# Performance work log

Measured on AMD Instinct MI355X. Metric: run time of the kernel, lower is better.

Reference implementation:

```python
import jax, jax.numpy as jnp
import numpy as np

NUM_TAGS = 256
BATCH = 64
SEQ = 512


def setup_inputs() -> dict:
    key = jax.random.key(0)
    k1, k2, k3 = jax.random.split(key, 3)
    logits = jax.random.normal(k1, (BATCH, SEQ, NUM_TAGS), dtype=jnp.float32)
    tags = jax.random.randint(k2, (BATCH, SEQ), 0, NUM_TAGS, dtype=jnp.int32)
    mask = jnp.ones((BATCH, SEQ), dtype=jnp.int32)
    # learned parameter: transitions [K, K] (xavier-normal-ish init)
    std = float(np.sqrt(2.0 / (NUM_TAGS + NUM_TAGS)))
    transitions = jax.random.normal(k3, (NUM_TAGS, NUM_TAGS), dtype=jnp.float32) * std
    return {"logits": logits, "tags": tags, "mask": mask, "transitions": transitions}


def _input_likelihood(logits, mask, transitions):
    # logits: [B, S, K], mask: [B, S] float
    logits_t = jnp.transpose(logits, (1, 0, 2))  # [S, B, K]
    mask_t = jnp.transpose(mask, (1, 0))         # [S, B]
    alpha0 = logits_t[0]                          # [B, K]

    def step(alpha, xs):
        logit_i, mask_i = xs                      # [B, K], [B]
        # inner: [B, K_prev, K_next]
        inner = alpha[:, :, None] + logit_i[:, None, :] + transitions[None, :, :]
        new_alpha = jax.nn.logsumexp(inner, axis=1)
        m = mask_i[:, None]
        alpha = new_alpha * m + alpha * (1.0 - m)
        return alpha, None

    alpha, _ = jax.lax.scan(step, alpha0, (logits_t[1:], mask_t[1:]))
    return jax.nn.logsumexp(alpha, axis=-1)      # [B]


def _joint_likelihood(logits, tags, mask, transitions):
    # logits: [B, S, K], tags: [B, S] int, mask: [B, S] float
    B, S, K = logits.shape
    # transition scores for steps 0..S-2 -> transitions[tags[i], tags[i+1]] * mask[i+1]
    trans = transitions[tags[:, :-1], tags[:, 1:]] * mask[:, 1:]      # [B, S-1]
    # emit scores for steps 0..S-2 -> logits[i, tags[i]] * mask[i]
    emit = jnp.take_along_axis(logits[:, :-1], tags[:, :-1, None], axis=-1)[..., 0] * mask[:, :-1]
    score = trans.sum(axis=1) + emit.sum(axis=1)                      # [B]
    # last valid tag per batch (mask is a contiguous prefix)
    last_idx = mask.sum(axis=1).astype(jnp.int32) - 1                 # [B]
    last_tags = jnp.take_along_axis(tags, last_idx[:, None], axis=1)[:, 0]
    last_input = logits[:, -1, :][jnp.arange(B), last_tags]           # [B]
    score = score + last_input * mask[:, -1]
    return score


def reference(logits, tags, mask, transitions):
    mask_f = mask.astype(logits.dtype)
    log_num = _joint_likelihood(logits, tags, mask_f, transitions)
    log_den = _input_likelihood(logits, mask_f, transitions)
    return jnp.sum(log_num - log_den)
```

## Files before the change

kernel.cpp:

```cpp
#include <hip/hip_runtime.h>
#include <stdint.h>

#define NTAGS 256
#define BATCH 64
#define SEQ   512
#define MB    16
#define NTHREADS 512

typedef __attribute__((ext_vector_type(8))) short short8;
typedef __attribute__((ext_vector_type(4))) float f32x4;

__device__ __forceinline__ unsigned int f32_to_bf16_bits(float f) {
  unsigned int u = __float_as_uint(f);
  return (u + 0x7FFFu + ((u >> 16) & 1u)) >> 16;
}
__device__ __forceinline__ float wave_sum(float v) {
#pragma unroll
  for (int o = 32; o; o >>= 1) v += __shfl_xor(v, o);
  return v;
}
__device__ __forceinline__ unsigned int pk_bf16(float lo, float hi) {
  unsigned int r;
  asm("v_cvt_pk_bf16_f32 %0, %1, %2" : "=v"(r) : "v"(lo), "v"(hi));
  return r;
}

#define LOG2E 1.4426950408889634f

#define BAR_LGKM() \
    asm volatile("s_waitcnt lgkmcnt(0)" ::: "memory"); \
    __builtin_amdgcn_s_barrier(); \
    asm volatile("" ::: "memory");

#define MFMA_ALL(RB) \
    f32x4 acc0 = {0.f,0.f,0.f,0.f}, acc1 = {0.f,0.f,0.f,0.f}; \
    _Pragma("unroll") \
    for (int c = 0; c < 8; ++c) { \
      const short8 bf = *(const short8*)&alds[RB][bidxs[c]]; \
      acc0 = __builtin_amdgcn_mfma_f32_16x16x32_bf16(aF[0][c], bf, acc0, 0, 0, 0); \
      acc1 = __builtin_amdgcn_mfma_f32_16x16x32_bf16(aF[1][c], bf, acc1, 0, 0, 0); \
    }

#define EPI_TILE_F(I, ACCI, PB, WB, ME) { \
      const uint2 pw = PB[I]; \
      const float p0_ = __uint_as_float(pw.x << 16); \
      const float p1_ = __uint_as_float(pw.x & 0xFFFF0000u); \
      const float p2_ = __uint_as_float(pw.y << 16); \
      const float p3_ = __uint_as_float(pw.y & 0xFFFF0000u); \
      const float n0 = (MM ? ACCI[0] * p0_ : sOld[I][0]) * sc; \
      const float n1 = (MM ? ACCI[1] * p1_ : sOld[I][1]) * sc; \
      const float n2 = (MM ? ACCI[2] * p2_ : sOld[I][2]) * sc; \
      const float n3 = (MM ? ACCI[3] * p3_ : sOld[I][3]) * sc; \
      sOld[I][0] = n0; sOld[I][1] = n1; sOld[I][2] = n2; sOld[I][3] = n3; \
      if (ME) mxl = fmaxf(mxl, fmaxf(fmaxf(n0, n1), fmaxf(n2, n3))); \
      uint2 wv; wv.x = pk_bf16(n0, n1); wv.y = pk_bf16(n2, n3); \
      *(uint2*)&alds[WB][widx[I]] = wv; }

#define EPI_TILE_B(I, ACCI, PB, WB, ME) { \
      const uint2 pw = PB[I]; \
      const float p0_ = __uint_as_float(pw.x << 16); \
      const float p1_ = __uint_as_float(pw.x & 0xFFFF0000u); \
      const float p2_ = __uint_as_float(pw.y << 16); \
      const float p3_ = __uint_as_float(pw.y & 0xFFFF0000u); \
      float n0, n1, n2, n3; \
      if (fastm) { \
        n0 = ACCI[0] * p0_ * sc; n1 = ACCI[1] * p1_ * sc; \
        n2 = ACCI[2] * p2_ * sc; n3 = ACCI[3] * p3_ * sc; \
      } else { \
        const float q0_ = __uint_as_float(gp[I].x << 16); \
        const float q1_ = __uint_as_float(gp[I].x & 0xFFFF0000u); \
        const float q2_ = __uint_as_float(gp[I].y << 16); \
        const float q3_ = __uint_as_float(gp[I].y & 0xFFFF0000u); \
        n0 = (MM ? ACCI[0] * p0_ : sOld[I][0] * (p0_ / q0_)) * sc; \
        n1 = (MM ? ACCI[1] * p1_ : sOld[I][1] * (p1_ / q1_)) * sc; \
        n2 = (MM ? ACCI[2] * p2_ : sOld[I][2] * (p2_ / q2_)) * sc; \
        n3 = (MM ? ACCI[3] * p3_ : sOld[I][3] * (p3_ / q3_)) * sc; \
      } \
      gp[I] = pw; \
      sOld[I][0] = n0; sOld[I][1] = n1; sOld[I][2] = n2; sOld[I][3] = n3; \
      if (ME) mxl = fmaxf(mxl, fmaxf(fmaxf(n0, n1), fmaxf(n2, n3))); \
      uint2 wv; wv.x = pk_bf16(n0, n1); wv.y = pk_bf16(n2, n3); \
      *(uint2*)&alds[WB][widx[I]] = wv; }

#define APPLY_BODY() { \
      const f32x4 mxa = *(const f32x4*)&maxw[p][0]; \
      const f32x4 mxb = *(const f32x4*)&maxw[p][4]; \
      const float mx = fmaxf(fmaxf(fmaxf(mxa[0], mxa[1]), fmaxf(mxa[2], mxa[3])), \
                             fmaxf(fmaxf(mxb[0], mxb[1]), fmaxf(mxb[2], mxb[3]))); \
      const int e = (int)((__float_as_uint(mx) >> 23) & 0xFF) - 127; \
      esum += e; \
      sc = __uint_as_float((unsigned int)(127 - e) << 23); }

#define STEPF(T, RB, WB, PC, PL, MC, ML, APPLY, MEAS) { \
    { const int tp_ = ((T) + 2 < SEQ) ? ((T) + 2) : (SEQ - 1); \
      _Pragma("unroll") \
      for (int i2 = 0; i2 < 2; ++i2) PL[i2] = *(const uint2*)(Pp + (size_t)tp_ * NTAGS + 16 * i2); \
      ML = mkp[tp_]; } \
    MFMA_ALL(RB) \
    float sc = 1.0f; \
    if (APPLY) APPLY_BODY() \
    const int MM = MC; \
    float mxl = -3.0e38f; \
    EPI_TILE_F(0, acc0, PC, WB, MEAS) EPI_TILE_F(1, acc1, PC, WB, MEAS) \
    if (MEAS) { \
      float v = mxl; v = fmaxf(v, __shfl_xor(v, 16)); v = fmaxf(v, __shfl_xor(v, 32)); \
      if (q == 0) maxw[p][wid] = v; \
    } \
    BAR_LGKM() }

#define STEPB(T, RB, WB, PC, PL, MC, ML, APPLY, MEAS) { \
    { const int tp_ = ((T) >= 2) ? ((T) - 2) : 0; \
      const int tm_ = ((T) >= 1) ? ((T) - 1) : 0; \
      _Pragma("unroll") \
      for (int i2 = 0; i2 < 2; ++i2) PL[i2] = *(const uint2*)(Pp + (size_t)tp_ * NTAGS + 16 * i2); \
      ML = mkp[tm_]; } \
    MFMA_ALL(RB) \
    float sc = 1.0f; \
    if (APPLY) APPLY_BODY() \
    const int MM = MC; \
    const bool fastm = (bool)__all(MM != 0); \
    float mxl = -3.0e38f; \
    EPI_TILE_B(0, acc0, PC, WB, MEAS) EPI_TILE_B(1, acc1, PC, WB, MEAS) \
    if (MEAS) { \
      float v = mxl; v = fmaxf(v, __shfl_xor(v, 16)); v = fmaxf(v, __shfl_xor(v, 32)); \
      if (q == 0) maxw[p][wid] = v; \
    } \
    BAR_LGKM() }

__global__ __launch_bounds__(256)
void crf_prep(const float* __restrict__ lg, unsigned int* __restrict__ P)
{
  const size_t g = (size_t)blockIdx.x * 256 + threadIdx.x;
  const float4 a = ((const float4*)lg)[2 * g];
  const float4 b = ((const float4*)lg)[2 * g + 1];
  uint4 o;
  o.x = pk_bf16(exp2f(a.x * LOG2E), exp2f(a.y * LOG2E));
  o.y = pk_bf16(exp2f(a.z * LOG2E), exp2f(a.w * LOG2E));
  o.z = pk_bf16(exp2f(b.x * LOG2E), exp2f(b.y * LOG2E));
  o.w = pk_bf16(exp2f(b.z * LOG2E), exp2f(b.w * LOG2E));
  ((uint4*)P)[g] = o;
}

__global__ __launch_bounds__(NTHREADS, 2)
void crf_halves(const unsigned short* __restrict__ P,
                const int*   __restrict__ mask,
                const float* __restrict__ trans,
                float* __restrict__ wsA, float* __restrict__ wsB,
                int* __restrict__ wseF, int* __restrict__ wseB)
{
  const int bid  = blockIdx.x;
  const int bwd  = bid >> 2;
  const int b0   = (bid & 3) * MB;
  const int tid  = threadIdx.x;
  const int wid  = tid >> 6;
  const int lane = tid & 63;
  const int p    = lane & 15;
  const int q    = lane >> 4;

  __shared__ __align__(16) short alds[2][NTAGS * MB];
  __shared__ __align__(32) float maxw[16][8];

  const unsigned short* Pp = P + (size_t)(b0 + p) * SEQ * NTAGS + 32 * wid + 4 * q;
  const int* mkp = mask + (b0 + p) * SEQ;

  int bidxs[8], widx[2];
#pragma unroll
  for (int c = 0; c < 8; ++c) bidxs[c] = (p * NTAGS + 32 * c + 8 * q) ^ ((p & 7) << 3);
#pragma unroll
  for (int i = 0; i < 2; ++i) widx[i] = (p * NTAGS + 32 * wid + 16 * i + 4 * q) ^ ((p & 7) << 3);

  short8 aF[2][8];
#pragma unroll
  for (int i = 0; i < 2; ++i) {
    const int m = 32 * wid + 16 * i + p;
#pragma unroll
    for (int c = 0; c < 8; ++c) {
      short8 w;
#pragma unroll
      for (int j = 0; j < 8; ++j) {
        const int tag = 32 * c + 8 * q + j;
        const float tv = bwd ? trans[m * NTAGS + tag] : trans[tag * NTAGS + m];
        w[j] = (short)f32_to_bf16_bits(exp2f(tv * LOG2E));
      }
      aF[i][c] = w;
    }
  }

  f32x4 sOld[2];
  uint2 p0[2], p1[2], p2[2], p3[2], gp[2];
  int m0 = 1, m1 = 1, m2 = 1, m3 = 1;
  int esum = 0;

  if (!bwd) {
#pragma unroll
    for (int i = 0; i < 2; ++i) {
      const uint2 pw = *(const uint2*)(Pp + 16 * i);
      f32x4 a;
      a[0] = __uint_as_float(pw.x << 16); a[1] = __uint_as_float(pw.x & 0xFFFF0000u);
      a[2] = __uint_as_float(pw.y << 16); a[3] = __uint_as_float(pw.y & 0xFFFF0000u);
      sOld[i] = a;
      *(uint2*)&alds[0][widx[i]] = pw;
    }
#pragma unroll
    for (int i = 0; i < 2; ++i) {
      p1[i] = *(const uint2*)(Pp + 1 * NTAGS + 16 * i);
      p2[i] = *(const uint2*)(Pp + 2 * NTAGS + 16 * i);
    }
    m1 = mkp[1]; m2 = mkp[2];
    __syncthreads();

    STEPF(1, 0, 1, p1, p3, m1, m3, 0, 0)
    STEPF(2, 1, 0, p2, p0, m2, m0, 0, 0)
    STEPF(3, 0, 1, p3, p1, m3, m1, 0, 1)
#pragma unroll 1
    for (int tb = 4; tb <= 248; tb += 4) {
      STEPF(tb + 0, 1, 0, p0, p2, m0, m2, 1, 0)
      STEPF(tb + 1, 0, 1, p1, p3, m1, m3, 0, 0)
      STEPF(tb + 2, 1, 0, p2, p0, m2, m0, 0, 0)
      STEPF(tb + 3, 0, 1, p3, p1, m3, m1, 0, 1)
    }
    STEPF(252, 1, 0, p0, p2, m0, m2, 1, 0)
    STEPF(253, 0, 1, p1, p3, m1, m3, 0, 0)
    STEPF(254, 1, 0, p2, p0, m2, m0, 0, 0)

    {
      MFMA_ALL(0)
      const int MM = m3;
      float* wp = wsA + (size_t)(b0 + p) * NTAGS + 32 * wid + 4 * q;
#pragma unroll
      for (int i = 0; i < 2; ++i) {
        const uint2 pw = p3[i];
        f32x4 pv;
        pv[0] = __uint_as_float(pw.x << 16); pv[1] = __uint_as_float(pw.x & 0xFFFF0000u);
        pv[2] = __uint_as_float(pw.y << 16); pv[3] = __uint_as_float(pw.y & 0xFFFF0000u);
        f32x4 o;
        const f32x4 ac = (i == 0) ? acc0 : acc1;
#pragma unroll
        for (int r = 0; r < 4; ++r)
          o[r] = MM ? ac[r] * pv[r] : sOld[i][r];
        *(f32x4*)(wp + 16 * i) = o;
      }
    }
    if (tid < 16) wseF[b0 + tid] = esum;
  } else {
#pragma unroll
    for (int i = 0; i < 2; ++i) {
      const uint2 pw = *(const uint2*)(Pp + (size_t)(SEQ - 1) * NTAGS + 16 * i);
      f32x4 a;
      a[0] = __uint_as_float(pw.x << 16); a[1] = __uint_as_float(pw.x & 0xFFFF0000u);
      a[2] = __uint_as_float(pw.y << 16); a[3] = __uint_as_float(pw.y & 0xFFFF0000u);
      sOld[i] = a; gp[i] = pw;
      *(uint2*)&alds[0][widx[i]] = pw;
    }
#pragma unroll
    for (int i = 0; i < 2; ++i) {
      p2[i] = *(const uint2*)(Pp + (size_t)510 * NTAGS + 16 * i);
      p1[i] = *(const uint2*)(Pp + (size_t)509 * NTAGS + 16 * i);
    }
    m2 = mkp[511];
    m1 = mkp[510];
    __syncthreads();

    STEPB(510, 0, 1, p2, p0, m2, m0, 0, 0)
    STEPB(509, 1, 0, p1, p3, m1, m3, 0, 0)
    STEPB(508, 0, 1, p0, p2, m0, m2, 0, 1)
#pragma unroll 1
    for (int tb = 507; tb >= 263; tb -= 4) {
      STEPB(tb - 0, 1, 0, p3, p1, m3, m1, 1, 0)
      STEPB(tb - 1, 0, 1, p2, p0, m2, m0, 0, 0)
      STEPB(tb - 2, 1, 0, p1, p3, m1, m3, 0, 0)
      STEPB(tb - 3, 0, 1, p0, p2, m0, m2, 0, 1)
    }
    STEPB(259, 1, 0, p3, p1, m3, m1, 1, 0)
    STEPB(258, 0, 1, p2, p0, m2, m0, 0, 0)
    STEPB(257, 1, 0, p1, p3, m1, m3, 0, 0)
    STEPB(256, 0, 1, p0, p2, m0, m2, 0, 0)

    {
      MFMA_ALL(1)
      float* wp = wsB + (size_t)(b0 + p) * NTAGS + 32 * wid + 4 * q;
      *(f32x4*)(wp + 0)  = acc0;
      *(f32x4*)(wp + 16) = acc1;
    }
    if (tid < 16) wseB[b0 + tid] = esum;
  }
}

__global__ __launch_bounds__(256)
void crf_combine(const float* __restrict__ logits,
                 const int*   __restrict__ tags,
                 const int*   __restrict__ mask,
                 const float* __restrict__ trans,
                 const float* __restrict__ wsA,
                 const float* __restrict__ wsB,
                 const int*   __restrict__ wseF,
                 const int*   __restrict__ wseB,
                 float* __restrict__ out)
{
  const int b    = blockIdx.x;
  const int tid  = threadIdx.x;
  const int lane = tid & 63;
  const int wid  = tid >> 6;

  __shared__ float rn[4], rm[4], rp[4];

  const float LN2 = 0.6931471805599453f;
  const float* lg = logits + (size_t)b * SEQ * NTAGS;
  const int*   tg = tags + b * SEQ;
  const int*   mk = mask + b * SEQ;

  float numer = 0.f, msum = 0.f;
  for (int t = tid; t < SEQ; t += 256) {
    int   tag_t = tg[t];
    float m_t   = (float)mk[t];
    msum += m_t;
    if (t < SEQ - 1) {
      numer += lg[t * NTAGS + tag_t] * m_t;
      numer += trans[tag_t * NTAGS + tg[t + 1]] * (float)mk[t + 1];
    }
  }
  numer = wave_sum(numer);
  msum  = wave_sum(msum);
  if (lane == 0) { rn[wid] = numer; rm[wid] = msum; }

  float pprod = wsA[b * NTAGS + tid] * wsB[b * NTAGS + tid];
  pprod = wave_sum(pprod);
  if (lane == 0) rp[wid] = pprod;
  __syncthreads();

  if (tid == 0) {
    const float numer_tot = (rn[0] + rn[1]) + (rn[2] + rn[3]);
    const float msum_tot  = (rm[0] + rm[1]) + (rm[2] + rm[3]);
    const float psum      = (rp[0] + rp[1]) + (rp[2] + rp[3]);
    const float log_den   = logf(psum) + (float)(wseF[b] + wseB[b]) * LN2;
    int last_idx = (int)msum_tot - 1;
    if (last_idx < 0) last_idx = 0;
    const int last_tag = tg[last_idx];
    const float score = numer_tot + lg[(SEQ - 1) * NTAGS + last_tag] * (float)mk[SEQ - 1];
    atomicAdd(out, score - log_den);
  }
}

extern "C" void kernel_launch(void* const* d_in, const int* in_sizes, int n_in,
                              void* d_out, int out_size, void* d_ws, size_t ws_size,
                              hipStream_t stream) {
  const float* logits = (const float*)d_in[0];
  const int*   tags   = (const int*)d_in[1];
  const int*   mask   = (const int*)d_in[2];
  const float* trans  = (const float*)d_in[3];
  float* out = (float*)d_out;

  unsigned short* P = (unsigned short*)d_ws;
  float* wsA  = (float*)((char*)d_ws + (size_t)BATCH * SEQ * NTAGS * 2);
  float* wsB  = wsA + BATCH * NTAGS;
  int*   wseF = (int*)(wsB + BATCH * NTAGS);
  int*   wseB = wseF + BATCH;

  hipMemsetAsync(out, 0, sizeof(float), stream);
  crf_prep<<<dim3(BATCH * SEQ * NTAGS / (256 * 8)), dim3(256), 0, stream>>>(logits, (unsigned int*)P);
  crf_halves<<<dim3(8), dim3(NTHREADS), 0, stream>>>(P, mask, trans, wsA, wsB, wseF, wseB);
  crf_combine<<<dim3(BATCH), dim3(256), 0, stream>>>(logits, tags, mask, trans, wsA, wsB, wseF, wseB, out);
}
```

Baseline: 280.1 us.

## Split recurrence across more blocks with four batch rows per block

Each crf_halves block now handles 4 batch rows instead of 16, so the launch grows from 8 to 32 blocks. Inside the 16-wide MFMA N dimension the rows are replicated, and only lanes with p<4 write LDS, the max buffer and outputs. The LDS swizzle is adapted to the smaller buffer. The aim is to shorten the latency-bound sequential chain per block by using more CUs, at the cost of redundant MFMA work and loading the transition matrix in more blocks.

```diff
diff --git a/kernel.cpp b/kernel.cpp
--- a/kernel.cpp
+++ b/kernel.cpp
@@ -4,7 +4,7 @@
 #define NTAGS 256
 #define BATCH 64
 #define SEQ   512
-#define MB    16
+#define BR    4
 #define NTHREADS 512
 
 typedef __attribute__((ext_vector_type(8))) short short8;
@@ -54,7 +54,7 @@
       sOld[I][0] = n0; sOld[I][1] = n1; sOld[I][2] = n2; sOld[I][3] = n3; \
       if (ME) mxl = fmaxf(mxl, fmaxf(fmaxf(n0, n1), fmaxf(n2, n3))); \
       uint2 wv; wv.x = pk_bf16(n0, n1); wv.y = pk_bf16(n2, n3); \
-      *(uint2*)&alds[WB][widx[I]] = wv; }
+      if (wrt) *(uint2*)&alds[WB][widx[I]] = wv; }
 
 #define EPI_TILE_B(I, ACCI, PB, WB, ME) { \
       const uint2 pw = PB[I]; \
@@ -80,11 +80,11 @@
       sOld[I][0] = n0; sOld[I][1] = n1; sOld[I][2] = n2; sOld[I][3] = n3; \
       if (ME) mxl = fmaxf(mxl, fmaxf(fmaxf(n0, n1), fmaxf(n2, n3))); \
       uint2 wv; wv.x = pk_bf16(n0, n1); wv.y = pk_bf16(n2, n3); \
-      *(uint2*)&alds[WB][widx[I]] = wv; }
+      if (wrt) *(uint2*)&alds[WB][widx[I]] = wv; }
 
 #define APPLY_BODY() { \
-      const f32x4 mxa = *(const f32x4*)&maxw[p][0]; \
-      const f32x4 mxb = *(const f32x4*)&maxw[p][4]; \
+      const f32x4 mxa = *(const f32x4*)&maxw[pc][0]; \
+      const f32x4 mxb = *(const f32x4*)&maxw[pc][4]; \
       const float mx = fmaxf(fmaxf(fmaxf(mxa[0], mxa[1]), fmaxf(mxa[2], mxa[3])), \
                              fmaxf(fmaxf(mxb[0], mxb[1]), fmaxf(mxb[2], mxb[3]))); \
       const int e = (int)((__float_as_uint(mx) >> 23) & 0xFF) - 127; \
@@ -104,7 +104,7 @@
     EPI_TILE_F(0, acc0, PC, WB, MEAS) EPI_TILE_F(1, acc1, PC, WB, MEAS) \
     if (MEAS) { \
       float v = mxl; v = fmaxf(v, __shfl_xor(v, 16)); v = fmaxf(v, __shfl_xor(v, 32)); \
-      if (q == 0) maxw[p][wid] = v; \
+      if (q == 0 && wrt) maxw[p][wid] = v; \
     } \
     BAR_LGKM() }
 
@@ -123,7 +123,7 @@
     EPI_TILE_B(0, acc0, PC, WB, MEAS) EPI_TILE_B(1, acc1, PC, WB, MEAS) \
     if (MEAS) { \
       float v = mxl; v = fmaxf(v, __shfl_xor(v, 16)); v = fmaxf(v, __shfl_xor(v, 32)); \
-      if (q == 0) maxw[p][wid] = v; \
+      if (q == 0 && wrt) maxw[p][wid] = v; \
     } \
     BAR_LGKM() }
 
@@ -149,25 +149,27 @@
                 int* __restrict__ wseF, int* __restrict__ wseB)
 {
   const int bid  = blockIdx.x;
-  const int bwd  = bid >> 2;
-  const int b0   = (bid & 3) * MB;
+  const int bwd  = bid >> 4;
+  const int b0   = (bid & 15) * BR;
   const int tid  = threadIdx.x;
   const int wid  = tid >> 6;
   const int lane = tid & 63;
   const int p    = lane & 15;
+  const int pc   = p & (BR - 1);
   const int q    = lane >> 4;
-
-  __shared__ __align__(16) short alds[2][NTAGS * MB];
-  __shared__ __align__(32) float maxw[16][8];
-
-  const unsigned short* Pp = P + (size_t)(b0 + p) * SEQ * NTAGS + 32 * wid + 4 * q;
-  const int* mkp = mask + (b0 + p) * SEQ;
+  const bool wrt = (p < BR);
+
+  __shared__ __align__(16) short alds[2][NTAGS * BR];
+  __shared__ __align__(32) float maxw[BR][8];
+
+  const unsigned short* Pp = P + (size_t)(b0 + pc) * SEQ * NTAGS + 32 * wid + 4 * q;
+  const int* mkp = mask + (b0 + pc) * SEQ;
 
   int bidxs[8], widx[2];
 #pragma unroll
-  for (int c = 0; c < 8; ++c) bidxs[c] = (p * NTAGS + 32 * c + 8 * q) ^ ((p & 7) << 3);
-#pragma unroll
-  for (int i = 0; i < 2; ++i) widx[i] = (p * NTAGS + 32 * wid + 16 * i + 4 * q) ^ ((p & 7) << 3);
+  for (int c = 0; c < 8; ++c) bidxs[c] = (pc * NTAGS + 32 * c + 8 * q) ^ ((pc & 1) << 5);
+#pragma unroll
+  for (int i = 0; i < 2; ++i) widx[i] = (p * NTAGS + 32 * wid + 16 * i + 4 * q) ^ ((p & 1) << 5);
 
   short8 aF[2][8];
 #pragma unroll
@@ -199,7 +201,7 @@
       a[0] = __uint_as_float(pw.x << 16); a[1] = __uint_as_float(pw.x & 0xFFFF0000u);
       a[2] = __uint_as_float(pw.y << 16); a[3] = __uint_as_float(pw.y & 0xFFFF0000u);
       sOld[i] = a;
-      *(uint2*)&alds[0][widx[i]] = pw;
+      if (wrt) *(uint2*)&alds[0][widx[i]] = pw;
     }
 #pragma unroll
     for (int i = 0; i < 2; ++i) {
@@ -226,7 +228,7 @@
     {
       MFMA_ALL(0)
       const int MM = m3;
-      float* wp = wsA + (size_t)(b0 + p) * NTAGS + 32 * wid + 4 * q;
+      float* wp = wsA + (size_t)(b0 + pc) * NTAGS + 32 * wid + 4 * q;
 #pragma unroll
       for (int i = 0; i < 2; ++i) {
         const uint2 pw = p3[i];
@@ -238,10 +240,10 @@
 #pragma unroll
         for (int r = 0; r < 4; ++r)
           o[r] = MM ? ac[r] * pv[r] : sOld[i][r];
-        *(f32x4*)(wp + 16 * i) = o;
+        if (wrt) *(f32x4*)(wp + 16 * i) = o;
       }
     }
-    if (tid < 16) wseF[b0 + tid] = esum;
+    if (tid < BR) wseF[b0 + tid] = esum;
   } else {
 #pragma unroll
     for (int i = 0; i < 2; ++i) {
@@ -250,7 +252,7 @@
       a[0] = __uint_as_float(pw.x << 16); a[1] = __uint_as_float(pw.x & 0xFFFF0000u);
       a[2] = __uint_as_float(pw.y << 16); a[3] = __uint_as_float(pw.y & 0xFFFF0000u);
       sOld[i] = a; gp[i] = pw;
-      *(uint2*)&alds[0][widx[i]] = pw;
+      if (wrt) *(uint2*)&alds[0][widx[i]] = pw;
     }
 #pragma unroll
     for (int i = 0; i < 2; ++i) {
@@ -278,11 +280,13 @@
 
     {
       MFMA_ALL(1)
-      float* wp = wsB + (size_t)(b0 + p) * NTAGS + 32 * wid + 4 * q;
-      *(f32x4*)(wp + 0)  = acc0;
-      *(f32x4*)(wp + 16) = acc1;
-    }
-    if (tid < 16) wseB[b0 + tid] = esum;
+      float* wp = wsB + (size_t)(b0 + pc) * NTAGS + 32 * wid + 4 * q;
+      if (wrt) {
+        *(f32x4*)(wp + 0)  = acc0;
+        *(f32x4*)(wp + 16) = acc1;
+      }
+    }
+    if (tid < BR) wseB[b0 + tid] = esum;
   }
 }
 
@@ -358,6 +362,6 @@
 
   hipMemsetAsync(out, 0, sizeof(float), stream);
   crf_prep<<<dim3(BATCH * SEQ * NTAGS / (256 * 8)), dim3(256), 0, stream>>>(logits, (unsigned int*)P);
-  crf_halves<<<dim3(8), dim3(NTHREADS), 0, stream>>>(P, mask, trans, wsA, wsB, wseF, wseB);
+  crf_halves<<<dim3(32), dim3(NTHREADS), 0, stream>>>(P, mask, trans, wsA, wsB, wseF, wseB);
   crf_combine<<<dim3(BATCH), dim3(256), 0, stream>>>(logits, tags, mask, trans, wsA, wsB, wseF, wseB, out);
 }
```

Result: faster. 241.0 us (-14.0%).
